# Performance work log

Measured on AMD Instinct MI355X. Metric: run time of the kernel, lower is better.

## Reference

```python
import jax, jax.numpy as jnp
import numpy as np

N_USERS = 50000
N_ITEMS = 30000
NNZ = 1_600_000
EMBED = 128
ATT = 128
TAU = 0.5


def setup_inputs() -> dict:
    key = jax.random.key(0)
    ks = jax.random.split(key, 9)
    user_embed = jax.random.normal(ks[0], (N_USERS, EMBED), dtype=jnp.float32)
    item_embed = jax.random.normal(ks[1], (N_ITEMS, EMBED), dtype=jnp.float32)
    Wq = jax.random.normal(ks[2], (ATT, EMBED), dtype=jnp.float32) * (1.0 / np.sqrt(EMBED))
    bq = jnp.zeros((ATT,), dtype=jnp.float32)
    Wk = jax.random.normal(ks[3], (ATT, EMBED), dtype=jnp.float32) * (1.0 / np.sqrt(EMBED))
    bk = jnp.zeros((ATT,), dtype=jnp.float32)
    adj_vals = jnp.ones((NNZ,), dtype=jnp.float32)
    gumbel_u_ui = jax.random.uniform(ks[4], (NNZ,), dtype=jnp.float32, minval=1e-10, maxval=1.0)
    gumbel_u_iu = jax.random.uniform(ks[5], (NNZ,), dtype=jnp.float32, minval=1e-10, maxval=1.0)
    rows = jax.random.randint(ks[6], (NNZ,), 0, N_USERS, dtype=jnp.int32)
    cols = jax.random.randint(ks[7], (NNZ,), 0, N_ITEMS, dtype=jnp.int32)
    return dict(user_embed=user_embed, item_embed=item_embed, Wq=Wq, bq=bq, Wk=Wk, bk=bk,
                adj_vals=adj_vals, gumbel_u_ui=gumbel_u_ui, gumbel_u_iu=gumbel_u_iu,
                rows=rows, cols=cols)


def _segment_softmax(vals, seg, num_segments):
    # numerically stable softmax over edges grouped by segment id (sparse row softmax)
    m = jax.ops.segment_max(vals, seg, num_segments=num_segments)
    e = jnp.exp(vals - m[seg])
    s = jax.ops.segment_sum(e, seg, num_segments=num_segments)
    return e / s[seg]


def reference(user_embed, item_embed, Wq, bq, Wk, bk, adj_vals, gumbel_u_ui, gumbel_u_iu, rows, cols):
    # ---- M_ui = sparse_softmax_rows( (adj * (Q(u) @ K(i).T) - G) / tau ) on edge support ----
    Qu = user_embed @ Wq.T + bq          # [U, A]
    Ki = item_embed @ Wk.T + bk          # [I, A]
    # edge-wise dot: equals dense (Qu @ Ki.T)[rows, cols] without materializing [U, I]
    w_ui = adj_vals * jnp.einsum('ed,ed->e', Qu[rows], Ki[cols])
    g_ui = jnp.log(-jnp.log(gumbel_u_ui))
    ui_vals = _segment_softmax((w_ui - g_ui) / TAU, rows, N_USERS)
    # ---- M_iu: transpose adjacency, Q over items, K over users, row-softmax over items ----
    Qi = item_embed @ Wq.T + bq          # [I, A]
    Ku = user_embed @ Wk.T + bk          # [U, A]
    w_iu = adj_vals * jnp.einsum('ed,ed->e', Qi[cols], Ku[rows])
    g_iu = jnp.log(-jnp.log(gumbel_u_iu))
    iu_vals = _segment_softmax((w_iu - g_iu) / TAU, cols, N_ITEMS)
    # block mask [[0, M_ui], [M_iu, 0]]: pads contribute nothing, so the nonzero
    # values of the concatenated mask are exactly these two edge-value arrays.
    return jnp.stack([ui_vals, iu_vals])  # [2, NNZ]
```

## Files before the change

kernel.cpp:

```cpp
#include <hip/hip_runtime.h>
#include <hip/hip_bf16.h>


#define EMB 128
#define TAUINV 2.0f
#define LOG2E 1.44269504f
#define CAP 128
#define OCAP 65536
#define NSCAT 2048

__device__ __forceinline__ unsigned fkey(float f) {
    unsigned u = __float_as_uint(f);
    return (u & 0x80000000u) ? ~u : (u | 0x80000000u);
}
__device__ __forceinline__ float fdecode(unsigned u) {
    return __uint_as_float((u & 0x80000000u) ? (u ^ 0x80000000u) : ~u);
}

__device__ __forceinline__ double dexp_fast(float lg) {
    float t = lg * LOG2E;
    float kf = floorf(t);
    float f = exp2f(t - kf);
    return ldexp((double)f, (int)kf);
}

__global__ void k_prep(const float* __restrict__ Wq, const float* __restrict__ Wk,
                       const float* __restrict__ bq, const float* __restrict__ bk,
                       float* __restrict__ BIGM, float* __restrict__ v1,
                       float* __restrict__ v2, float* __restrict__ c0) {
    int e1 = blockIdx.x, e2 = threadIdx.x;
    float acc = 0.f;
    for (int a = 0; a < EMB; ++a) acc += Wq[a * EMB + e1] * Wk[a * EMB + e2];
    BIGM[e2 * 256 + e1] = acc;
    BIGM[e1 * 256 + 128 + e2] = acc;
    if (e2 == 0) { float s = 0.f; for (int a = 0; a < EMB; ++a) s += Wq[a * EMB + e1] * bk[a]; v1[e1] = s; }
    if (e2 == 1) { float s = 0.f; for (int a = 0; a < EMB; ++a) s += Wk[a * EMB + e1] * bq[a]; v2[e1] = s; }
    if (e1 == 0 && e2 == 2) { float s = 0.f; for (int a = 0; a < EMB; ++a) s += bq[a] * bk[a]; c0[0] = s; }
    if (e1 == 0 && e2 == 3) { float s = 0.f; for (int a = 0; a < EMB; ++a) s += fabsf(bq[a]) + fabsf(bk[a]); c0[1] = s; }
}

__global__ void k_rowdot2(const float* __restrict__ Xu, const float* __restrict__ Xi,
                          int U, int I,
                          const float* __restrict__ v1, const float* __restrict__ v2,
                          float2* __restrict__ t12, float2* __restrict__ u12) {
    int g = blockIdx.x * 8 + (threadIdx.x >> 5);
    int l = threadIdx.x & 31;
    if (g >= U + I) return;
    const float* X = (g < U) ? (Xu + (size_t)g * EMB) : (Xi + (size_t)(g - U) * EMB);
    float4 x = ((const float4*)X)[l];
    float4 av = ((const float4*)v1)[l];
    float4 bv = ((const float4*)v2)[l];
    float pa = x.x * av.x + x.y * av.y + x.z * av.z + x.w * av.w;
    float pb = x.x * bv.x + x.y * bv.y + x.z * bv.z + x.w * bv.w;
    for (int off = 16; off; off >>= 1) { pa += __shfl_xor(pa, off); pb += __shfl_xor(pb, off); }
    if (l == 0) {
        if (g < U) t12[g] = make_float2(pa, pb);
        else       u12[g - U] = make_float2(pb, pa);
    }
}

__global__ __launch_bounds__(256) void k_mid(
    const float* __restrict__ Xi, const float* __restrict__ BIGM,
    float* __restrict__ CD, int nItems, int nbCD,
    const int* __restrict__ rows, const int* __restrict__ cols,
    const float* __restrict__ adj, const float* __restrict__ gu1,
    const float* __restrict__ gu2,
    const float2* __restrict__ t12, const float2* __restrict__ u12,
    const float* __restrict__ c0p, int nnz,
    unsigned* __restrict__ cnt, int4* __restrict__ SA,
    float* __restrict__ SB, int* __restrict__ OV,
    unsigned* __restrict__ ovfc) {
    __shared__ float Xs[32][EMB];
    __shared__ float Ms[32][256];
    if (blockIdx.x < (unsigned)nbCD) {
        const int t = threadIdx.x;
        const int m0 = blockIdx.x * 32;

        const float4* Xi4 = (const float4*)Xi;
        float4* Xs4 = (float4*)Xs;
        for (int idx = t; idx < 32 * 32; idx += 256) {
            int r = idx >> 5, c = idx & 31;
            int row = m0 + r;
            Xs4[idx] = (row < nItems) ? Xi4[(size_t)row * 32 + c]
                                      : make_float4(0.f, 0.f, 0.f, 0.f);
        }

        const int tc = t & 63;
        const int tr = t >> 6;
        float4 acc[8] = {};

        const float4* BG4 = (const float4*)BIGM;
        float4* Ms4 = (float4*)Ms;
        for (int kc = 0; kc < EMB; kc += 32) {
            __syncthreads();
            for (int idx = t; idx < 32 * 64; idx += 256)
                Ms4[idx] = BG4[(size_t)(kc + (idx >> 6)) * 64 + (idx & 63)];
            __syncthreads();
#pragma unroll
            for (int kk = 0; kk < 32; ++kk) {
                float4 w = Ms4[kk * 64 + tc];
#pragma unroll
                for (int i = 0; i < 8; ++i) {
                    float x = Xs[tr * 8 + i][kc + kk];
                    acc[i].x += x * w.x; acc[i].y += x * w.y;
                    acc[i].z += x * w.z; acc[i].w += x * w.w;
                }
            }
        }
#pragma unroll
        for (int i = 0; i < 8; ++i) {
            int row = m0 + tr * 8 + i;
            if (row < nItems)
                ((float4*)(CD + (size_t)row * 256))[tc] = acc[i];
        }
    } else {
        const float c0 = c0p[0];
        const bool useb = (c0p[1] != 0.f);
        int i = (blockIdx.x - nbCD) * blockDim.x + threadIdx.x;
        int st = NSCAT * blockDim.x;
        for (int e = i; e < nnz; e += st) {
            int r = rows[e], c = cols[e];
            unsigned pos = atomicAdd(&cnt[c], 1u);
            float a = adj[e];
            float g1 = logf(-logf(gu1[e]));
            float g2 = logf(-logf(gu2[e]));
            float b1 = -g1 * TAUINV;
            float b2 = -g2 * TAUINV;
            if (useb) {
                float2 tt = t12[r];
                float2 uu = u12[c];
                b1 += a * (tt.x + uu.x + c0) * TAUINV;
                b2 += a * (tt.y + uu.y + c0) * TAUINV;
            }
            if (pos < CAP) {
                size_t s = (size_t)c * CAP + pos;
                SA[s] = make_int4(r, e, __float_as_int(a * TAUINV), __float_as_int(b1));
                SB[s] = b2;
            } else {
                unsigned o = atomicAdd(ovfc, 1u);
                if (o < OCAP) {
                    int* p = OV + (size_t)o * 6;
                    p[0] = r; p[1] = c; p[2] = e;
                    p[3] = __float_as_int(a * TAUINV);
                    p[4] = __float_as_int(b1); p[5] = __float_as_int(b2);
                }
            }
        }
    }
}

__global__ __launch_bounds__(256) void k_edge14(
    const float* __restrict__ Xu, const float* __restrict__ CD,
    const unsigned* __restrict__ cnt, const int4* __restrict__ SA,
    const float* __restrict__ SB,
    float2* __restrict__ L12, double* __restrict__ s1d, double* __restrict__ s2d,
    int I) {
    const int g = threadIdx.x >> 4, l = threadIdx.x & 15;
    const int c = blockIdx.x * 16 + g;
    if (c >= I) return;
    unsigned n = cnt[c]; if (n > CAP) n = CAP;
    if (n == 0) return;
    const unsigned lo = (unsigned)c * CAP;
    const unsigned hi = lo + n;
    const float4* cd = (const float4*)(CD + (size_t)c * 256);
    const float4 cv0 = cd[l], cv1 = cd[l + 16];
    const float4 dv0 = cd[l + 32], dv1 = cd[l + 48];
    double s2acc = 0.0;
    for (unsigned j = lo; j < hi; ++j) {
        int4 m = SA[j];
        float b2s = SB[j];
        const float4* xu = (const float4*)(Xu + (size_t)m.x * EMB);
        float4 x0 = xu[l], x1 = xu[l + 16];
        float p1 = x0.x * cv0.x + x0.y * cv0.y + x0.z * cv0.z + x0.w * cv0.w
                 + x1.x * cv1.x + x1.y * cv1.y + x1.z * cv1.z + x1.w * cv1.w;
        float p2 = x0.x * dv0.x + x0.y * dv0.y + x0.z * dv0.z + x0.w * dv0.w
                 + x1.x * dv1.x + x1.y * dv1.y + x1.z * dv1.z + x1.w * dv1.w;
#pragma unroll
        for (int off = 1; off < 16; off <<= 1) {
            p1 += __shfl_xor(p1, off);
            p2 += __shfl_xor(p2, off);
        }
        if (l < 2) {
            float aP = __int_as_float(m.z);
            float bP = (l == 0) ? __int_as_float(m.w) : b2s;
            float lg = fmaf(aP, (l == 0) ? p1 : p2, bP);
            double ev = dexp_fast(lg);
            ((float*)(L12 + m.y))[l] = lg;
            if (l == 0) unsafeAtomicAdd(s1d + m.x, ev);
            else        s2acc += ev;
        }
    }
    if (l == 1) s2d[c] = s2acc;
}

__global__ void k_ovf(const float* __restrict__ Xu, const float* __restrict__ CD,
                      const int* __restrict__ OV, const unsigned* __restrict__ ovfc,
                      float2* __restrict__ L12, double* __restrict__ s1d,
                      double* __restrict__ s2d) {
    int n = (int)*ovfc; if (n > OCAP) n = OCAP;
    if (n == 0) return;
    const int gid = (blockIdx.x * blockDim.x + threadIdx.x) >> 4;
    const int ng = (gridDim.x * blockDim.x) >> 4;
    const int l = threadIdx.x & 15;
    for (int i = gid; i < n; i += ng) {
        const int* p = OV + (size_t)i * 6;
        int r = p[0], c = p[1], e = p[2];
        const float4* xu = (const float4*)(Xu + (size_t)r * EMB);
        const float4* cd = (const float4*)(CD + (size_t)c * 256);
        float4 x0 = xu[l], x1 = xu[l + 16];
        float4 cv0 = cd[l], cv1 = cd[l + 16];
        float4 dv0 = cd[l + 32], dv1 = cd[l + 48];
        float p1 = x0.x * cv0.x + x0.y * cv0.y + x0.z * cv0.z + x0.w * cv0.w
                 + x1.x * cv1.x + x1.y * cv1.y + x1.z * cv1.z + x1.w * cv1.w;
        float p2 = x0.x * dv0.x + x0.y * dv0.y + x0.z * dv0.z + x0.w * dv0.w
                 + x1.x * dv1.x + x1.y * dv1.y + x1.z * dv1.z + x1.w * dv1.w;
#pragma unroll
        for (int off = 1; off < 16; off <<= 1) {
            p1 += __shfl_xor(p1, off);
            p2 += __shfl_xor(p2, off);
        }
        if (l < 2) {
            float aP = __int_as_float(p[3]);
            float bP = __int_as_float((l == 0) ? p[4] : p[5]);
            float lg = fmaf(aP, (l == 0) ? p1 : p2, bP);
            double ev = dexp_fast(lg);
            ((float*)(L12 + e))[l] = lg;
            if (l == 0) unsafeAtomicAdd(s1d + r, ev);
            else        unsafeAtomicAdd(s2d + c, ev);
        }
    }
}

__global__ void k_ls(const double* __restrict__ s1d, const double* __restrict__ s2d,
                     float* __restrict__ ls1, float* __restrict__ ls2, int U, int I) {
    int i = blockIdx.x * blockDim.x + threadIdx.x;
    if (i >= U + I) return;
    double s = (i < U) ? s1d[i] : s2d[i - U];
    int ex;
    double m = frexp(s, &ex);
    float l2 = log2f((float)m) + (float)ex;
    if (i < U) ls1[i] = l2; else ls2[i - U] = l2;
}

__global__ void k_fin4(const int* __restrict__ rows, const int* __restrict__ cols,
                       const float2* __restrict__ L12,
                       const float* __restrict__ ls1, const float* __restrict__ ls2,
                       float* __restrict__ out, int nnz) {
    int i = blockIdx.x * blockDim.x + threadIdx.x, st = gridDim.x * blockDim.x;
    for (int e = i; e < nnz; e += st) {
        float2 lg = L12[e];
        out[e]       = exp2f(fmaf(lg.x, LOG2E, -ls1[rows[e]]));
        out[nnz + e] = exp2f(fmaf(lg.y, LOG2E, -ls2[cols[e]]));
    }
}

__global__ __launch_bounds__(256) void k_cd(const float* __restrict__ Xi,
                                            const float* __restrict__ BIGM,
                                            float* __restrict__ CD, int nItems) {
    __shared__ float Xs[32][EMB];
    __shared__ float Ms[32][256];
    const int t = threadIdx.x;
    const int m0 = blockIdx.x * 32;
    const float4* Xi4 = (const float4*)Xi;
    float4* Xs4 = (float4*)Xs;
    for (int idx = t; idx < 32 * 32; idx += 256) {
        int r = idx >> 5, c = idx & 31;
        int row = m0 + r;
        Xs4[idx] = (row < nItems) ? Xi4[(size_t)row * 32 + c]
                                  : make_float4(0.f, 0.f, 0.f, 0.f);
    }
    const int tc = t & 63;
    const int tr = t >> 6;
    float4 acc[8] = {};
    const float4* BG4 = (const float4*)BIGM;
    float4* Ms4 = (float4*)Ms;
    for (int kc = 0; kc < EMB; kc += 32) {
        __syncthreads();
        for (int idx = t; idx < 32 * 64; idx += 256)
            Ms4[idx] = BG4[(size_t)(kc + (idx >> 6)) * 64 + (idx & 63)];
        __syncthreads();
#pragma unroll
        for (int kk = 0; kk < 32; ++kk) {
            float4 w = Ms4[kk * 64 + tc];
#pragma unroll
            for (int i = 0; i < 8; ++i) {
                float x = Xs[tr * 8 + i][kc + kk];
                acc[i].x += x * w.x; acc[i].y += x * w.y;
                acc[i].z += x * w.z; acc[i].w += x * w.w;
            }
        }
    }
#pragma unroll
    for (int i = 0; i < 8; ++i) {
        int row = m0 + tr * 8 + i;
        if (row < nItems)
            ((float4*)(CD + (size_t)row * 256))[tc] = acc[i];
    }
}

__global__ __launch_bounds__(256) void k_edge1(
    const float* __restrict__ Xu, const float* __restrict__ CD,
    const float2* __restrict__ t12, const float2* __restrict__ u12,
    const float* __restrict__ c0p, const float* __restrict__ adj,
    const float* __restrict__ gu1, const float* __restrict__ gu2,
    const int* __restrict__ rows, const int* __restrict__ cols,
    float* __restrict__ L1, float* __restrict__ L2,
    unsigned* __restrict__ mx1, unsigned* __restrict__ mx2, int nnz) {
    const int gid = blockIdx.x * 8 + (threadIdx.x >> 5);
    const int l = threadIdx.x & 31;
    const int stride = gridDim.x * 8;
    const float c0 = c0p[0];
    for (int e = gid; e < nnz; e += stride) {
        int r = rows[e], c = cols[e];
        float4 xu = ((const float4*)(Xu + (size_t)r * EMB))[l];
        const float4* cd = (const float4*)(CD + (size_t)c * 256);
        float4 cv = cd[l];
        float4 dv = cd[32 + l];
        float p1 = xu.x * cv.x + xu.y * cv.y + xu.z * cv.z + xu.w * cv.w;
        float p2 = xu.x * dv.x + xu.y * dv.y + xu.z * dv.z + xu.w * dv.w;
        for (int off = 16; off; off >>= 1) { p1 += __shfl_xor(p1, off); p2 += __shfl_xor(p2, off); }
        if (l < 2) {
            float p = (l == 0) ? p1 : p2;
            float2 tt = t12[r];
            float2 uu = u12[c];
            float tb = (l == 0) ? tt.x : tt.y;
            float ub = (l == 0) ? uu.x : uu.y;
            float g = logf(-logf(((l == 0) ? gu1 : gu2)[e]));
            float w = adj[e] * (p + tb + ub + c0);
            float lg = (w - g) * TAUINV;
            if (l == 0) { L1[e] = lg; atomicMax(mx1 + r, fkey(lg)); }
            else        { L2[e] = lg; atomicMax(mx2 + c, fkey(lg)); }
        }
    }
}

__global__ void k_sum(const int* __restrict__ rows, const int* __restrict__ cols,
                      const float* __restrict__ L1, const float* __restrict__ L2,
                      const unsigned* __restrict__ mx1, const unsigned* __restrict__ mx2,
                      float* __restrict__ s1, float* __restrict__ s2, int nnz) {
    int i = blockIdx.x * blockDim.x + threadIdx.x, st = gridDim.x * blockDim.x;
    for (int e = i; e < nnz; e += st) {
        int r = rows[e], c = cols[e];
        atomicAdd(s1 + r, expf(L1[e] - fdecode(mx1[r])));
        atomicAdd(s2 + c, expf(L2[e] - fdecode(mx2[c])));
    }
}

__global__ void k_fin2(const int* __restrict__ rows, const int* __restrict__ cols,
                       const float* __restrict__ L1, const float* __restrict__ L2,
                       const unsigned* __restrict__ mx1, const unsigned* __restrict__ mx2,
                       const float* __restrict__ s1, const float* __restrict__ s2,
                       float* __restrict__ out, int nnz) {
    int i = blockIdx.x * blockDim.x + threadIdx.x, st = gridDim.x * blockDim.x;
    for (int e = i; e < nnz; e += st) {
        int r = rows[e], c = cols[e];
        out[e]       = expf(L1[e] - fdecode(mx1[r])) / s1[r];
        out[nnz + e] = expf(L2[e] - fdecode(mx2[c])) / s2[c];
    }
}

extern "C" void kernel_launch(void* const* d_in, const int* in_sizes, int n_in,
                              void* d_out, int out_size, void* d_ws, size_t ws_size,
                              hipStream_t stream) {
    const float* Xu  = (const float*)d_in[0];
    const float* Xi  = (const float*)d_in[1];
    const float* Wq  = (const float*)d_in[2];
    const float* bq  = (const float*)d_in[3];
    const float* Wk  = (const float*)d_in[4];
    const float* bk  = (const float*)d_in[5];
    const float* adj = (const float*)d_in[6];
    const float* gu1 = (const float*)d_in[7];
    const float* gu2 = (const float*)d_in[8];
    const int* rows  = (const int*)d_in[9];
    const int* cols  = (const int*)d_in[10];
    float* out = (float*)d_out;

    const int U   = in_sizes[0] / EMB;
    const int I   = in_sizes[1] / EMB;
    const int nnz = in_sizes[6];
    const int nbCD = (I + 31) / 32;

    char* w = (char*)d_ws;
    size_t off_b = 0;
    auto alloc = [&](size_t bytes) {
        char* p = w + off_b;
        off_b += (bytes + 15) & ~(size_t)15;
        return p;
    };

    float* BIGM = (float*)alloc(32768 * 4);
    float* v1   = (float*)alloc(128 * 4);
    float* v2   = (float*)alloc(128 * 4);
    float* c0   = (float*)alloc(64 * 4);
    float2* t12 = (float2*)alloc((size_t)U * 8);
    float2* u12 = (float2*)alloc((size_t)I * 8);
    float* CD   = (float*)alloc((size_t)I * 256 * 4);
    float2* L12 = (float2*)alloc((size_t)nnz * 8);
    size_t base_need = off_b;
    double* s1d    = (double*)alloc((size_t)U * 8);
    unsigned* cnt  = (unsigned*)alloc((size_t)I * 4);
    unsigned* ovfc = (unsigned*)alloc(16 * 4);
    double* s2d    = (double*)alloc((size_t)I * 8);
    float* ls1     = (float*)alloc((size_t)U * 4);
    float* ls2     = (float*)alloc((size_t)I * 4);
    int4* SA = (int4*)alloc((size_t)I * CAP * 16);
    float* SB = (float*)alloc((size_t)I * CAP * 4);
    int* OV = (int*)alloc((size_t)OCAP * 24);
    size_t sorted_need = off_b;
    unsigned* mx1 = (unsigned*)alloc((size_t)U * 4);
    unsigned* mx2 = (unsigned*)alloc((size_t)I * 4);
    float* s1f  = (float*)alloc((size_t)U * 4);
    float* s2f  = (float*)alloc((size_t)I * 4);
    size_t fallback_need = off_b;

    const bool use_sorted = (sorted_need <= ws_size);
    if (!use_sorted && fallback_need > ws_size) return;

    k_prep<<<128, 128, 0, stream>>>(Wq, Wk, bq, bk, BIGM, v1, v2, c0);
    k_rowdot2<<<(U + I + 7) / 8, 256, 0, stream>>>(Xu, Xi, U, I, v1, v2, t12, u12);

    if (use_sorted) {
        (void)hipMemsetAsync(s1d, 0, (size_t)U * 8 + (size_t)I * 4 + 64, stream);
        k_mid<<<nbCD + NSCAT, 256, 0, stream>>>(Xi, BIGM, CD, I, nbCD,
                                                rows, cols, adj, gu1, gu2,
                                                t12, u12, c0, nnz, cnt, SA, SB,
                                                OV, ovfc);
        k_edge14<<<(I + 15) / 16, 256, 0, stream>>>(Xu, CD, cnt, SA, SB, L12,
                                                    s1d, s2d, I);
        k_ovf<<<64, 256, 0, stream>>>(Xu, CD, OV, ovfc, L12, s1d, s2d);
        k_ls<<<(U + I + 255) / 256, 256, 0, stream>>>(s1d, s2d, ls1, ls2, U, I);
        k_fin4<<<2048, 256, 0, stream>>>(rows, cols, L12, ls1, ls2, out, nnz);
    } else {
        float* L1 = (float*)L12;
        float* L2 = L1 + nnz;
        (void)hipMemsetAsync(mx1, 0, (size_t)(2 * (U + I)) * 4, stream);
        k_cd<<<nbCD, 256, 0, stream>>>(Xi, BIGM, CD, I);
        k_edge1<<<4096, 256, 0, stream>>>(Xu, CD, t12, u12, c0, adj, gu1, gu2,
                                          rows, cols, L1, L2, mx1, mx2, nnz);
        k_sum<<<2048, 256, 0, stream>>>(rows, cols, L1, L2, mx1, mx2, s1f, s2f, nnz);
        k_fin2<<<2048, 256, 0, stream>>>(rows, cols, L1, L2, mx1, mx2, s1f, s2f,
                                         out, nnz);
    }
}
```

Measured before the change: 359.0 us.

## Pack edge biases as half2 into SA, drop k_ls, skip rowdot when biases are zero

Stores the two per-edge bias terms as a packed half2 inside the int4 bucket entry, which removes the separate SB array and its write and read traffic. Removes the k_ls log-sum kernel, so the final kernel divides by the double sums directly. Also makes k_rowdot2 and the fallback edge kernel skip the bias row-dot work when the biases are all zero. Half precision for the Gumbel-derived biases loses accuracy in the logits, and the double division in the final kernel is more expensive per edge.

```diff
diff --git a/kernel.cpp b/kernel.cpp
--- a/kernel.cpp
+++ b/kernel.cpp
@@ -1,5 +1,6 @@
 #include <hip/hip_runtime.h>
 #include <hip/hip_bf16.h>
+#include <hip/hip_fp16.h>
 
 
 #define EMB 128
@@ -42,7 +43,9 @@
 __global__ void k_rowdot2(const float* __restrict__ Xu, const float* __restrict__ Xi,
                           int U, int I,
                           const float* __restrict__ v1, const float* __restrict__ v2,
+                          const float* __restrict__ c0p,
                           float2* __restrict__ t12, float2* __restrict__ u12) {
+    if (c0p[1] == 0.f) return;
     int g = blockIdx.x * 8 + (threadIdx.x >> 5);
     int l = threadIdx.x & 31;
     if (g >= U + I) return;
@@ -68,8 +71,7 @@
     const float2* __restrict__ t12, const float2* __restrict__ u12,
     const float* __restrict__ c0p, int nnz,
     unsigned* __restrict__ cnt, int4* __restrict__ SA,
-    float* __restrict__ SB, int* __restrict__ OV,
-    unsigned* __restrict__ ovfc) {
+    int* __restrict__ OV, unsigned* __restrict__ ovfc) {
     __shared__ float Xs[32][EMB];
     __shared__ float Ms[32][256];
     if (blockIdx.x < (unsigned)nbCD) {
@@ -133,9 +135,10 @@
                 b2 += a * (tt.y + uu.y + c0) * TAUINV;
             }
             if (pos < CAP) {
-                size_t s = (size_t)c * CAP + pos;
-                SA[s] = make_int4(r, e, __float_as_int(a * TAUINV), __float_as_int(b1));
-                SB[s] = b2;
+                __half2 hb = __floats2half2_rn(b1, b2);
+                SA[(size_t)c * CAP + pos] =
+                    make_int4(r, e, __float_as_int(a * TAUINV),
+                              *(const int*)&hb);
             } else {
                 unsigned o = atomicAdd(ovfc, 1u);
                 if (o < OCAP) {
@@ -152,7 +155,6 @@
 __global__ __launch_bounds__(256) void k_edge14(
     const float* __restrict__ Xu, const float* __restrict__ CD,
     const unsigned* __restrict__ cnt, const int4* __restrict__ SA,
-    const float* __restrict__ SB,
     float2* __restrict__ L12, double* __restrict__ s1d, double* __restrict__ s2d,
     int I) {
     const int g = threadIdx.x >> 4, l = threadIdx.x & 15;
@@ -168,7 +170,6 @@
     double s2acc = 0.0;
     for (unsigned j = lo; j < hi; ++j) {
         int4 m = SA[j];
-        float b2s = SB[j];
         const float4* xu = (const float4*)(Xu + (size_t)m.x * EMB);
         float4 x0 = xu[l], x1 = xu[l + 16];
         float p1 = x0.x * cv0.x + x0.y * cv0.y + x0.z * cv0.z + x0.w * cv0.w
@@ -181,8 +182,9 @@
             p2 += __shfl_xor(p2, off);
         }
         if (l < 2) {
+            __half2 hb = *(const __half2*)&m.w;
             float aP = __int_as_float(m.z);
-            float bP = (l == 0) ? __int_as_float(m.w) : b2s;
+            float bP = (l == 0) ? __low2float(hb) : __high2float(hb);
             float lg = fmaf(aP, (l == 0) ? p1 : p2, bP);
             double ev = dexp_fast(lg);
             ((float*)(L12 + m.y))[l] = lg;
@@ -231,26 +233,15 @@
     }
 }
 
-__global__ void k_ls(const double* __restrict__ s1d, const double* __restrict__ s2d,
-                     float* __restrict__ ls1, float* __restrict__ ls2, int U, int I) {
-    int i = blockIdx.x * blockDim.x + threadIdx.x;
-    if (i >= U + I) return;
-    double s = (i < U) ? s1d[i] : s2d[i - U];
-    int ex;
-    double m = frexp(s, &ex);
-    float l2 = log2f((float)m) + (float)ex;
-    if (i < U) ls1[i] = l2; else ls2[i - U] = l2;
-}
-
-__global__ void k_fin4(const int* __restrict__ rows, const int* __restrict__ cols,
+__global__ void k_fin5(const int* __restrict__ rows, const int* __restrict__ cols,
                        const float2* __restrict__ L12,
-                       const float* __restrict__ ls1, const float* __restrict__ ls2,
+                       const double* __restrict__ s1d, const double* __restrict__ s2d,
                        float* __restrict__ out, int nnz) {
     int i = blockIdx.x * blockDim.x + threadIdx.x, st = gridDim.x * blockDim.x;
     for (int e = i; e < nnz; e += st) {
         float2 lg = L12[e];
-        out[e]       = exp2f(fmaf(lg.x, LOG2E, -ls1[rows[e]]));
-        out[nnz + e] = exp2f(fmaf(lg.y, LOG2E, -ls2[cols[e]]));
+        out[e]       = (float)(dexp_fast(lg.x) / s1d[rows[e]]);
+        out[nnz + e] = (float)(dexp_fast(lg.y) / s2d[cols[e]]);
     }
 }
 
@@ -310,6 +301,7 @@
     const int l = threadIdx.x & 31;
     const int stride = gridDim.x * 8;
     const float c0 = c0p[0];
+    const bool useb = (c0p[1] != 0.f);
     for (int e = gid; e < nnz; e += stride) {
         int r = rows[e], c = cols[e];
         float4 xu = ((const float4*)(Xu + (size_t)r * EMB))[l];
@@ -321,10 +313,13 @@
         for (int off = 16; off; off >>= 1) { p1 += __shfl_xor(p1, off); p2 += __shfl_xor(p2, off); }
         if (l < 2) {
             float p = (l == 0) ? p1 : p2;
-            float2 tt = t12[r];
-            float2 uu = u12[c];
-            float tb = (l == 0) ? tt.x : tt.y;
-            float ub = (l == 0) ? uu.x : uu.y;
+            float tb = 0.f, ub = 0.f;
+            if (useb) {
+                float2 tt = t12[r];
+                float2 uu = u12[c];
+                tb = (l == 0) ? tt.x : tt.y;
+                ub = (l == 0) ? uu.x : uu.y;
+            }
             float g = logf(-logf(((l == 0) ? gu1 : gu2)[e]));
             float w = adj[e] * (p + tb + ub + c0);
             float lg = (w - g) * TAUINV;
@@ -401,10 +396,7 @@
     unsigned* cnt  = (unsigned*)alloc((size_t)I * 4);
     unsigned* ovfc = (unsigned*)alloc(16 * 4);
     double* s2d    = (double*)alloc((size_t)I * 8);
-    float* ls1     = (float*)alloc((size_t)U * 4);
-    float* ls2     = (float*)alloc((size_t)I * 4);
     int4* SA = (int4*)alloc((size_t)I * CAP * 16);
-    float* SB = (float*)alloc((size_t)I * CAP * 4);
     int* OV = (int*)alloc((size_t)OCAP * 24);
     size_t sorted_need = off_b;
     unsigned* mx1 = (unsigned*)alloc((size_t)U * 4);
@@ -417,19 +409,19 @@
     if (!use_sorted && fallback_need > ws_size) return;
 
     k_prep<<<128, 128, 0, stream>>>(Wq, Wk, bq, bk, BIGM, v1, v2, c0);
-    k_rowdot2<<<(U + I + 7) / 8, 256, 0, stream>>>(Xu, Xi, U, I, v1, v2, t12, u12);
+    k_rowdot2<<<(U + I + 7) / 8, 256, 0, stream>>>(Xu, Xi, U, I, v1, v2, c0,
+                                                   t12, u12);
 
     if (use_sorted) {
         (void)hipMemsetAsync(s1d, 0, (size_t)U * 8 + (size_t)I * 4 + 64, stream);
         k_mid<<<nbCD + NSCAT, 256, 0, stream>>>(Xi, BIGM, CD, I, nbCD,
                                                 rows, cols, adj, gu1, gu2,
-                                                t12, u12, c0, nnz, cnt, SA, SB,
+                                                t12, u12, c0, nnz, cnt, SA,
                                                 OV, ovfc);
-        k_edge14<<<(I + 15) / 16, 256, 0, stream>>>(Xu, CD, cnt, SA, SB, L12,
+        k_edge14<<<(I + 15) / 16, 256, 0, stream>>>(Xu, CD, cnt, SA, L12,
                                                     s1d, s2d, I);
         k_ovf<<<64, 256, 0, stream>>>(Xu, CD, OV, ovfc, L12, s1d, s2d);
-        k_ls<<<(U + I + 255) / 256, 256, 0, stream>>>(s1d, s2d, ls1, ls2, U, I);
-        k_fin4<<<2048, 256, 0, stream>>>(rows, cols, L12, ls1, ls2, out, nnz);
+        k_fin5<<<2048, 256, 0, stream>>>(rows, cols, L12, s1d, s2d, out, nnz);
     } else {
         float* L1 = (float*)L12;
         float* L2 = L1 + nnz;
```

New measurement: 335.4 us. -6.6%, faster.
